# Performance work log

Hardware: AMD Instinct MI355X
Metric: run time of the kernel (lower is better)

Reference implementation:

```python
import jax, jax.numpy as jnp
import numpy as np

N_NODES = 50000
N_EDGES = 800000
IN_FEATS, H_FEATS, N_CLASSES = 64, 64, 16


def setup_inputs() -> dict:
    key = jax.random.key(0)
    ks = jax.random.split(key, 8)
    x = jax.random.normal(ks[0], (N_NODES, IN_FEATS), dtype=jnp.float32)
    src = jax.random.randint(ks[1], (N_EDGES,), 0, N_NODES, dtype=jnp.int64)
    dst = jax.random.randint(ks[2], (N_EDGES,), 0, N_NODES, dtype=jnp.int64)
    W_self1 = jax.random.normal(ks[3], (IN_FEATS, H_FEATS), dtype=jnp.float32) / np.sqrt(IN_FEATS)
    W_neigh1 = jax.random.normal(ks[4], (IN_FEATS, H_FEATS), dtype=jnp.float32) / np.sqrt(IN_FEATS)
    b1 = jnp.zeros((H_FEATS,), dtype=jnp.float32)
    W_self2 = jax.random.normal(ks[5], (H_FEATS, N_CLASSES), dtype=jnp.float32) / np.sqrt(H_FEATS)
    W_neigh2 = jax.random.normal(ks[6], (H_FEATS, N_CLASSES), dtype=jnp.float32) / np.sqrt(H_FEATS)
    b2 = jnp.zeros((N_CLASSES,), dtype=jnp.float32)
    return {"x": x, "src": src, "dst": dst,
            "W_self1": W_self1, "W_neigh1": W_neigh1, "b1": b1,
            "W_self2": W_self2, "W_neigh2": W_neigh2, "b2": b2}


def _mean_agg(h, src, dst, n_nodes):
    # gather source-node features along edges, sum into destinations, divide by in-degree
    summed = jax.ops.segment_sum(h[src], dst, num_segments=n_nodes)  # [N, d]
    deg = jax.ops.segment_sum(jnp.ones_like(src, dtype=h.dtype), dst, num_segments=n_nodes)
    return summed / jnp.maximum(deg, 1.0)[:, None]  # zero in-degree -> zeros (DGL semantics)


def _sage_layer(h, src, dst, W_self, W_neigh, b):
    h_neigh = _mean_agg(h, src, dst, h.shape[0])
    return h @ W_self + h_neigh @ W_neigh + b


def reference(x, src, dst, W_self1, W_neigh1, b1, W_self2, W_neigh2, b2):
    h = _sage_layer(x, src, dst, W_self1, W_neigh1, b1)
    h = jax.nn.relu(h)
    out = _sage_layer(h, src, dst, W_self2, W_neigh2, b2)
    return out
```

## Files before the change

### kernel.cpp

```cpp
#include <hip/hip_runtime.h>
#include <hip/hip_bf16.h>
#include <cstring>


#define FEATS 64
#define CLS   16
#define EPT   16
#define CAP   5120

typedef unsigned short bf16_t;
typedef float floatx2 __attribute__((ext_vector_type(2)));

__device__ __forceinline__ float bfbits2f(unsigned lo16) {
    unsigned v = lo16 << 16;
    float f;
    __builtin_memcpy(&f, &v, 4);
    return f;
}
__device__ __forceinline__ bf16_t f2bf(float f) {
    unsigned u;
    __builtin_memcpy(&u, &f, 4);
    u = (u + 0x7FFFu + ((u >> 16) & 1u)) >> 16;
    return (bf16_t)u;
}
__device__ __forceinline__ unsigned pack2(float a, float b) {
    return (unsigned)f2bf(a) | ((unsigned)f2bf(b) << 16);
}
__device__ __forceinline__ unsigned pack4_fp8(float a, float b, float c, float d) {
    int q = __builtin_amdgcn_cvt_pk_fp8_f32(a, b, 0, false);
    q = __builtin_amdgcn_cvt_pk_fp8_f32(c, d, q, true);
    return (unsigned)q;
}

__global__ __launch_bounds__(256) void fused_pg_kernel(
    const int* __restrict__ src, const int* __restrict__ dst,
    int* __restrict__ bucket_cnt, int* __restrict__ epart, int E,
    const float* __restrict__ x, const float* __restrict__ Ws,
    const float* __restrict__ Wn, bf16_t* __restrict__ selfo,
    unsigned char* __restrict__ t1, int N, int nbp)
{
    __shared__ float smem[16512];
    int t = threadIdx.x;

    if ((int)blockIdx.x < nbp) {
        int* hist = (int*)smem;
        int* base = hist + 256;
        int e0 = blockIdx.x * (256 * EPT);
        hist[t] = 0;
        __syncthreads();
        int pk[EPT];
        int bk[EPT];
#pragma unroll
        for (int j = 0; j < EPT; ++j) {
            int e = e0 + j * 256 + t;
            if (e < E) {
                int d = dst[e];
                pk[j] = (src[e] << 8) | (d & 255);
                bk[j] = d >> 8;
                atomicAdd(&hist[bk[j]], 1);
            } else bk[j] = -1;
        }
        __syncthreads();
        int c = hist[t];
        if (c) base[t] = atomicAdd(&bucket_cnt[t], c);
        hist[t] = 0;
        __syncthreads();
#pragma unroll
        for (int j = 0; j < EPT; ++j) {
            if (bk[j] >= 0) {
                int r = atomicAdd(&hist[bk[j]], 1);
                epart[bk[j] * CAP + base[bk[j]] + r] = pk[j];
            }
        }
        return;
    }

    float* Wc = smem;
    float* xs = smem + 8192;
    int node0 = ((int)blockIdx.x - nbp) * 128;

    for (int idx = t; idx < 64 * 128; idx += 256) {
        int k = idx >> 7, c = idx & 127;
        Wc[idx] = (c < 64) ? Ws[k * 64 + c] : Wn[k * 64 + (c - 64)];
    }
    for (int idx = t; idx < 128 * 16; idx += 256) {
        int row = idx >> 4, c4 = idx & 15;
        int node = node0 + row;
        float4 v = (node < N) ? ((const float4*)(x + (size_t)node * 64))[c4]
                              : make_float4(0.f, 0.f, 0.f, 0.f);
        float* p = &xs[row * 65 + c4 * 4];
        p[0] = v.x; p[1] = v.y; p[2] = v.z; p[3] = v.w;
    }
    __syncthreads();

    int m = t & 31;
    int g = t >> 5;
    float acc[4][16];
#pragma unroll
    for (int j = 0; j < 4; ++j)
#pragma unroll
        for (int c = 0; c < 16; ++c) acc[j][c] = 0.f;

    for (int k = 0; k < 64; ++k) {
        float w[16];
        const float* wp = &Wc[k * 128 + g * 16];
#pragma unroll
        for (int c = 0; c < 16; ++c) w[c] = wp[c];
        float a0 = xs[m * 65 + k];
        float a1 = xs[(m + 32) * 65 + k];
        float a2 = xs[(m + 64) * 65 + k];
        float a3 = xs[(m + 96) * 65 + k];
#pragma unroll
        for (int c = 0; c < 16; ++c) {
            acc[0][c] += a0 * w[c];
            acc[1][c] += a1 * w[c];
            acc[2][c] += a2 * w[c];
            acc[3][c] += a3 * w[c];
        }
    }
#pragma unroll
    for (int j = 0; j < 4; ++j) {
        int node = node0 + m + 32 * j;
        if (node < N) {
            if (g < 4) {
                bf16_t* dstp = selfo + (size_t)node * 64 + g * 16;
                uint4 p0, p1;
                p0.x = pack2(acc[j][0],  acc[j][1]);  p0.y = pack2(acc[j][2],  acc[j][3]);
                p0.z = pack2(acc[j][4],  acc[j][5]);  p0.w = pack2(acc[j][6],  acc[j][7]);
                p1.x = pack2(acc[j][8],  acc[j][9]);  p1.y = pack2(acc[j][10], acc[j][11]);
                p1.z = pack2(acc[j][12], acc[j][13]); p1.w = pack2(acc[j][14], acc[j][15]);
                *(uint4*)(dstp) = p0;
                *(uint4*)(dstp + 8) = p1;
            } else {
                unsigned char* dstp = t1 + (size_t)node * 64 + (g - 4) * 16;
                uint4 q;
                q.x = pack4_fp8(acc[j][0],  acc[j][1],  acc[j][2],  acc[j][3]);
                q.y = pack4_fp8(acc[j][4],  acc[j][5],  acc[j][6],  acc[j][7]);
                q.z = pack4_fp8(acc[j][8],  acc[j][9],  acc[j][10], acc[j][11]);
                q.w = pack4_fp8(acc[j][12], acc[j][13], acc[j][14], acc[j][15]);
                *(uint4*)(dstp) = q;
            }
        }
    }
}

__global__ __launch_bounds__(256) void buildcsr_kernel(const int* __restrict__ epart,
                                                       const int* __restrict__ bucket_cnt,
                                                       int* __restrict__ row_start,
                                                       unsigned short* __restrict__ deg16,
                                                       int* __restrict__ csr, int N) {
    __shared__ int cnt[256];
    __shared__ int pref[256];
    __shared__ int s[256];
    int t = threadIdx.x;
    int b = blockIdx.x;
    int ebeg = b * CAP;
    int ecnt = bucket_cnt[b];
    cnt[t] = 0;
    __syncthreads();
    for (int e = t; e < ecnt; e += 256)
        atomicAdd(&cnt[epart[ebeg + e] & 255], 1);
    __syncthreads();
    int v = cnt[t];
    s[t] = v;
    __syncthreads();
    for (int off = 1; off < 256; off <<= 1) {
        int u = (t >= off) ? s[t - off] : 0;
        __syncthreads();
        s[t] += u;
        __syncthreads();
    }
    pref[t] = s[t] - v;
    int node = b * 256 + t;
    if (node < N) {
        row_start[node] = ebeg + pref[t];
        deg16[node] = (unsigned short)v;
    }
    cnt[t] = 0;
    __syncthreads();
    for (int e = t; e < ecnt; e += 256) {
        int pk = epart[ebeg + e];
        int ln = pk & 255;
        int r = atomicAdd(&cnt[ln], 1);
        csr[ebeg + pref[ln] + r] = pk >> 8;
    }
}

__global__ __launch_bounds__(256) void gather64_kernel(
    const int* __restrict__ csr, const int* __restrict__ row_start,
    const unsigned short* __restrict__ deg16,
    const unsigned char* __restrict__ t1, const bf16_t* __restrict__ selfo,
    bf16_t* __restrict__ h1, const float* __restrict__ b1, int N)
{
    int wid = (blockIdx.x * 256 + threadIdx.x) >> 6;
    int lane = threadIdx.x & 63;
    int eslot = lane >> 4;
    int cg = lane & 15;
    if (wid >= N) return;
    int beg = row_start[wid];
    int d = deg16[wid];
    float ax = 0.f, ay = 0.f, az = 0.f, aw = 0.f;
    int i = eslot;
    for (; i + 12 < d; i += 16) {
        int s0 = csr[beg + i];
        int s1 = csr[beg + i + 4];
        int s2 = csr[beg + i + 8];
        int s3 = csr[beg + i + 12];
        unsigned r0 = *(const unsigned*)(t1 + (size_t)s0 * 64 + cg * 4);
        unsigned r1 = *(const unsigned*)(t1 + (size_t)s1 * 64 + cg * 4);
        unsigned r2 = *(const unsigned*)(t1 + (size_t)s2 * 64 + cg * 4);
        unsigned r3 = *(const unsigned*)(t1 + (size_t)s3 * 64 + cg * 4);
        floatx2 p0 = __builtin_amdgcn_cvt_pk_f32_fp8((int)r0, false);
        floatx2 q0 = __builtin_amdgcn_cvt_pk_f32_fp8((int)r0, true);
        floatx2 p1 = __builtin_amdgcn_cvt_pk_f32_fp8((int)r1, false);
        floatx2 q1 = __builtin_amdgcn_cvt_pk_f32_fp8((int)r1, true);
        floatx2 p2 = __builtin_amdgcn_cvt_pk_f32_fp8((int)r2, false);
        floatx2 q2 = __builtin_amdgcn_cvt_pk_f32_fp8((int)r2, true);
        floatx2 p3 = __builtin_amdgcn_cvt_pk_f32_fp8((int)r3, false);
        floatx2 q3 = __builtin_amdgcn_cvt_pk_f32_fp8((int)r3, true);
        ax += p0.x + p1.x + p2.x + p3.x;
        ay += p0.y + p1.y + p2.y + p3.y;
        az += q0.x + q1.x + q2.x + q3.x;
        aw += q0.y + q1.y + q2.y + q3.y;
    }
    for (; i < d; i += 4) {
        int s0 = csr[beg + i];
        unsigned r0 = *(const unsigned*)(t1 + (size_t)s0 * 64 + cg * 4);
        floatx2 p0 = __builtin_amdgcn_cvt_pk_f32_fp8((int)r0, false);
        floatx2 q0 = __builtin_amdgcn_cvt_pk_f32_fp8((int)r0, true);
        ax += p0.x; ay += p0.y; az += q0.x; aw += q0.y;
    }
    ax += __shfl_xor(ax, 16); ay += __shfl_xor(ay, 16);
    az += __shfl_xor(az, 16); aw += __shfl_xor(aw, 16);
    ax += __shfl_xor(ax, 32); ay += __shfl_xor(ay, 32);
    az += __shfl_xor(az, 32); aw += __shfl_xor(aw, 32);
    if (eslot == 0) {
        float inv = 1.f / fmaxf((float)d, 1.f);
        size_t o = (size_t)wid * 64 + cg * 4;
        uint2 su = *(const uint2*)(selfo + o);
        float4 bb = *(const float4*)(b1 + cg * 4);
        float rx = fmaxf(bfbits2f(su.x & 0xffff) + ax * inv + bb.x, 0.f);
        float ry = fmaxf(bfbits2f(su.x >> 16)    + ay * inv + bb.y, 0.f);
        float rz = fmaxf(bfbits2f(su.y & 0xffff) + az * inv + bb.z, 0.f);
        float rw = fmaxf(bfbits2f(su.y >> 16)    + aw * inv + bb.w, 0.f);
        uint2 pk;
        pk.x = pack2(rx, ry);
        pk.y = pack2(rz, rw);
        *(uint2*)(h1 + o) = pk;
    }
}

__global__ __launch_bounds__(256) void gemm2_kernel(
    const bf16_t* __restrict__ h1, const float* __restrict__ Ws,
    const float* __restrict__ Wn, float* __restrict__ outp,
    bf16_t* __restrict__ t2, int N)
{
    __shared__ float Wc[64 * 32];
    __shared__ float xs[128 * 65];
    int t = threadIdx.x;
    int node0 = blockIdx.x * 128;

    for (int idx = t; idx < 64 * 32; idx += 256) {
        int k = idx >> 5, c = idx & 31;
        Wc[idx] = (c < 16) ? Ws[k * 16 + c] : Wn[k * 16 + (c - 16)];
    }
    for (int idx = t; idx < 128 * 8; idx += 256) {
        int row = idx >> 3, c8 = idx & 7;
        int node = node0 + row;
        float* p = &xs[row * 65 + c8 * 8];
        if (node < N) {
            uint4 u = *(const uint4*)(h1 + (size_t)node * 64 + c8 * 8);
            p[0] = bfbits2f(u.x & 0xffff); p[1] = bfbits2f(u.x >> 16);
            p[2] = bfbits2f(u.y & 0xffff); p[3] = bfbits2f(u.y >> 16);
            p[4] = bfbits2f(u.z & 0xffff); p[5] = bfbits2f(u.z >> 16);
            p[6] = bfbits2f(u.w & 0xffff); p[7] = bfbits2f(u.w >> 16);
        } else {
            for (int qq = 0; qq < 8; ++qq) p[qq] = 0.f;
        }
    }
    __syncthreads();

    int m = t & 31;
    int g = t >> 5;
    float acc[4][4];
#pragma unroll
    for (int j = 0; j < 4; ++j)
#pragma unroll
        for (int c = 0; c < 4; ++c) acc[j][c] = 0.f;

    for (int k = 0; k < 64; ++k) {
        float w[4];
        const float* wp = &Wc[k * 32 + g * 4];
#pragma unroll
        for (int c = 0; c < 4; ++c) w[c] = wp[c];
        float a0 = xs[m * 65 + k];
        float a1 = xs[(m + 32) * 65 + k];
        float a2 = xs[(m + 64) * 65 + k];
        float a3 = xs[(m + 96) * 65 + k];
#pragma unroll
        for (int c = 0; c < 4; ++c) {
            acc[0][c] += a0 * w[c];
            acc[1][c] += a1 * w[c];
            acc[2][c] += a2 * w[c];
            acc[3][c] += a3 * w[c];
        }
    }
#pragma unroll
    for (int j = 0; j < 4; ++j) {
        int node = node0 + m + 32 * j;
        if (node < N) {
            if (g < 4) {
                *(float4*)(outp + (size_t)node * 16 + g * 4) =
                    make_float4(acc[j][0], acc[j][1], acc[j][2], acc[j][3]);
            } else {
                uint2 pk;
                pk.x = pack2(acc[j][0], acc[j][1]);
                pk.y = pack2(acc[j][2], acc[j][3]);
                *(uint2*)(t2 + (size_t)node * 16 + (g - 4) * 4) = pk;
            }
        }
    }
}

__global__ __launch_bounds__(256) void gather16_kernel(
    const int* __restrict__ csr, const int* __restrict__ row_start,
    const unsigned short* __restrict__ deg16,
    const bf16_t* __restrict__ t2,
    float* __restrict__ outp, const float* __restrict__ b2, int N)
{
    int gt = blockIdx.x * 256 + threadIdx.x;
    int node = gt >> 3;
    int c2 = gt & 7;
    if (node >= N) return;
    int beg = row_start[node];
    int d = deg16[node];
    int end = beg + d;
    float a0 = 0.f, a1 = 0.f;
    int i = beg;
    for (; i + 4 <= end; i += 4) {
        int s0 = csr[i], s1 = csr[i + 1], s2 = csr[i + 2], s3 = csr[i + 3];
        unsigned u0 = *(const unsigned*)(t2 + (size_t)s0 * 16 + c2 * 2);
        unsigned u1 = *(const unsigned*)(t2 + (size_t)s1 * 16 + c2 * 2);
        unsigned u2 = *(const unsigned*)(t2 + (size_t)s2 * 16 + c2 * 2);
        unsigned u3 = *(const unsigned*)(t2 + (size_t)s3 * 16 + c2 * 2);
        a0 += bfbits2f(u0 & 0xffff) + bfbits2f(u1 & 0xffff)
            + bfbits2f(u2 & 0xffff) + bfbits2f(u3 & 0xffff);
        a1 += bfbits2f(u0 >> 16) + bfbits2f(u1 >> 16)
            + bfbits2f(u2 >> 16) + bfbits2f(u3 >> 16);
    }
    for (; i < end; ++i) {
        int s = csr[i];
        unsigned u = *(const unsigned*)(t2 + (size_t)s * 16 + c2 * 2);
        a0 += bfbits2f(u & 0xffff);
        a1 += bfbits2f(u >> 16);
    }
    float inv = 1.f / fmaxf((float)d, 1.f);
    size_t o = (size_t)node * 16 + c2 * 2;
    outp[o]     += a0 * inv + b2[c2 * 2];
    outp[o + 1] += a1 * inv + b2[c2 * 2 + 1];
}

extern "C" void kernel_launch(void* const* d_in, const int* in_sizes, int n_in,
                              void* d_out, int out_size, void* d_ws, size_t ws_size,
                              hipStream_t stream) {
    const float* x   = (const float*)d_in[0];
    const int*   src = (const int*)d_in[1];
    const int*   dst = (const int*)d_in[2];
    const float* Ws1 = (const float*)d_in[3];
    const float* Wn1 = (const float*)d_in[4];
    const float* b1  = (const float*)d_in[5];
    const float* Ws2 = (const float*)d_in[6];
    const float* Wn2 = (const float*)d_in[7];
    const float* b2  = (const float*)d_in[8];
    float* outp = (float*)d_out;

    const int N = in_sizes[0] / FEATS;
    const int E = in_sizes[1];
    const int B = (N + 255) / 256;
    const int NBP = (E + 256 * EPT - 1) / (256 * EPT);
    const int NBG = (N + 127) / 128;

    char* p = (char*)d_ws;
    auto align16 = [](char* q) { return (char*)(((size_t)q + 15) & ~(size_t)15); };
    int* bucket_cnt    = (int*)p;                  p = (char*)(bucket_cnt + 256);
    int* epart         = (int*)p;                  p = (char*)(epart + (size_t)B * CAP);
    int* csr           = (int*)p;                  p = (char*)(csr + (size_t)B * CAP);
    int* row_start     = (int*)align16(p);         p = (char*)(row_start + N);
    unsigned short* deg16 = (unsigned short*)align16(p); p = (char*)(deg16 + N);
    bf16_t* selfo      = (bf16_t*)align16(p);      p = (char*)(selfo + (size_t)N * 64);
    unsigned char* t1  = (unsigned char*)align16(p); p = (char*)(t1 + (size_t)N * 64);
    bf16_t* h1         = (bf16_t*)align16(p);      p = (char*)(h1 + (size_t)N * 64);
    bf16_t* t2         = (bf16_t*)align16(p);

    hipMemsetAsync(bucket_cnt, 0, 256 * sizeof(int), stream);

    fused_pg_kernel<<<NBP + NBG, 256, 0, stream>>>(
        src, dst, bucket_cnt, epart, E, x, Ws1, Wn1, selfo, t1, N, NBP);
    buildcsr_kernel<<<B, 256, 0, stream>>>(epart, bucket_cnt, row_start, deg16, csr, N);

    gather64_kernel<<<((size_t)N * 64 + 255) / 256, 256, 0, stream>>>(
        csr, row_start, deg16, t1, selfo, h1, b1, N);
    gemm2_kernel<<<(N + 127) / 128, 256, 0, stream>>>(h1, Ws2, Wn2, outp, t2, N);
    gather16_kernel<<<((size_t)N * 8 + 255) / 256, 256, 0, stream>>>(
        csr, row_start, deg16, t2, outp, b2, N);
}
```

Measured before the change: 159.4 us.

## Branchless degree-specialized gathers and wavefront-per-node layer-2 aggregation

gather64 now handles degrees up to 16 and up to 32 with fully unrolled, clamped-index loads that are masked by a multiplier. This removes loop overhead and exposes all loads at once, since average in-degree is about 16. The self and bias loads are hoisted ahead of the gather so their latency overlaps it. gather16 is rewritten from 8 threads per node to a full 64-lane wavefront per node, with 8 edge slots and a shuffle reduction. That launches 8x more threads and leaves many lanes idle on the epilogue, in exchange for more memory-level parallelism.

Measured after the change: 155.0 us. 1.03x faster.

```diff
diff --git a/kernel.cpp b/kernel.cpp
--- a/kernel.cpp
+++ b/kernel.cpp
@@ -199,46 +199,87 @@
     if (wid >= N) return;
     int beg = row_start[wid];
     int d = deg16[wid];
+    size_t o = (size_t)wid * 64 + cg * 4;
+    uint2 su;
+    float4 bb;
+    if (eslot == 0) {
+        su = *(const uint2*)(selfo + o);
+        bb = *(const float4*)(b1 + cg * 4);
+    }
     float ax = 0.f, ay = 0.f, az = 0.f, aw = 0.f;
-    int i = eslot;
-    for (; i + 12 < d; i += 16) {
-        int s0 = csr[beg + i];
-        int s1 = csr[beg + i + 4];
-        int s2 = csr[beg + i + 8];
-        int s3 = csr[beg + i + 12];
-        unsigned r0 = *(const unsigned*)(t1 + (size_t)s0 * 64 + cg * 4);
-        unsigned r1 = *(const unsigned*)(t1 + (size_t)s1 * 64 + cg * 4);
-        unsigned r2 = *(const unsigned*)(t1 + (size_t)s2 * 64 + cg * 4);
-        unsigned r3 = *(const unsigned*)(t1 + (size_t)s3 * 64 + cg * 4);
-        floatx2 p0 = __builtin_amdgcn_cvt_pk_f32_fp8((int)r0, false);
-        floatx2 q0 = __builtin_amdgcn_cvt_pk_f32_fp8((int)r0, true);
-        floatx2 p1 = __builtin_amdgcn_cvt_pk_f32_fp8((int)r1, false);
-        floatx2 q1 = __builtin_amdgcn_cvt_pk_f32_fp8((int)r1, true);
-        floatx2 p2 = __builtin_amdgcn_cvt_pk_f32_fp8((int)r2, false);
-        floatx2 q2 = __builtin_amdgcn_cvt_pk_f32_fp8((int)r2, true);
-        floatx2 p3 = __builtin_amdgcn_cvt_pk_f32_fp8((int)r3, false);
-        floatx2 q3 = __builtin_amdgcn_cvt_pk_f32_fp8((int)r3, true);
-        ax += p0.x + p1.x + p2.x + p3.x;
-        ay += p0.y + p1.y + p2.y + p3.y;
-        az += q0.x + q1.x + q2.x + q3.x;
-        aw += q0.y + q1.y + q2.y + q3.y;
-    }
-    for (; i < d; i += 4) {
-        int s0 = csr[beg + i];
-        unsigned r0 = *(const unsigned*)(t1 + (size_t)s0 * 64 + cg * 4);
-        floatx2 p0 = __builtin_amdgcn_cvt_pk_f32_fp8((int)r0, false);
-        floatx2 q0 = __builtin_amdgcn_cvt_pk_f32_fp8((int)r0, true);
-        ax += p0.x; ay += p0.y; az += q0.x; aw += q0.y;
-    }
-    ax += __shfl_xor(ax, 16); ay += __shfl_xor(ay, 16);
-    az += __shfl_xor(az, 16); aw += __shfl_xor(aw, 16);
-    ax += __shfl_xor(ax, 32); ay += __shfl_xor(ay, 32);
-    az += __shfl_xor(az, 32); aw += __shfl_xor(aw, 32);
+    if (d > 0) {
+        int dm1 = d - 1;
+#define G64_ACC(r, m)                                                    \
+        {                                                                \
+            floatx2 p_ = __builtin_amdgcn_cvt_pk_f32_fp8((int)(r), false); \
+            floatx2 q_ = __builtin_amdgcn_cvt_pk_f32_fp8((int)(r), true);  \
+            ax += (m) * p_.x; ay += (m) * p_.y;                          \
+            az += (m) * q_.x; aw += (m) * q_.y;                          \
+        }
+        if (d <= 16) {
+            int i0 = eslot, i1 = eslot + 4, i2 = eslot + 8, i3 = eslot + 12;
+            int j0 = i0 > dm1 ? dm1 : i0;
+            int j1 = i1 > dm1 ? dm1 : i1;
+            int j2 = i2 > dm1 ? dm1 : i2;
+            int j3 = i3 > dm1 ? dm1 : i3;
+            int s0 = csr[beg + j0];
+            int s1 = csr[beg + j1];
+            int s2 = csr[beg + j2];
+            int s3 = csr[beg + j3];
+            unsigned r0 = *(const unsigned*)(t1 + (size_t)s0 * 64 + cg * 4);
+            unsigned r1 = *(const unsigned*)(t1 + (size_t)s1 * 64 + cg * 4);
+            unsigned r2 = *(const unsigned*)(t1 + (size_t)s2 * 64 + cg * 4);
+            unsigned r3 = *(const unsigned*)(t1 + (size_t)s3 * 64 + cg * 4);
+            float m0 = (i0 <= dm1) ? 1.f : 0.f;
+            float m1 = (i1 <= dm1) ? 1.f : 0.f;
+            float m2 = (i2 <= dm1) ? 1.f : 0.f;
+            float m3 = (i3 <= dm1) ? 1.f : 0.f;
+            G64_ACC(r0, m0); G64_ACC(r1, m1); G64_ACC(r2, m2); G64_ACC(r3, m3);
+        } else if (d <= 32) {
+            int idx[8];
+            float mk[8];
+            int ss[8];
+            unsigned rr[8];
+#pragma unroll
+            for (int k = 0; k < 8; ++k) {
+                int i = eslot + 4 * k;
+                idx[k] = i > dm1 ? dm1 : i;
+                mk[k] = (i <= dm1) ? 1.f : 0.f;
+            }
+#pragma unroll
+            for (int k = 0; k < 8; ++k) ss[k] = csr[beg + idx[k]];
+#pragma unroll
+            for (int k = 0; k < 8; ++k)
+                rr[k] = *(const unsigned*)(t1 + (size_t)ss[k] * 64 + cg * 4);
+#pragma unroll
+            for (int k = 0; k < 8; ++k) G64_ACC(rr[k], mk[k]);
+        } else {
+            int i = eslot;
+            for (; i + 12 < d; i += 16) {
+                int s0 = csr[beg + i];
+                int s1 = csr[beg + i + 4];
+                int s2 = csr[beg + i + 8];
+                int s3 = csr[beg + i + 12];
+                unsigned r0 = *(const unsigned*)(t1 + (size_t)s0 * 64 + cg * 4);
+                unsigned r1 = *(const unsigned*)(t1 + (size_t)s1 * 64 + cg * 4);
+                unsigned r2 = *(const unsigned*)(t1 + (size_t)s2 * 64 + cg * 4);
+                unsigned r3 = *(const unsigned*)(t1 + (size_t)s3 * 64 + cg * 4);
+                G64_ACC(r0, 1.f); G64_ACC(r1, 1.f); G64_ACC(r2, 1.f); G64_ACC(r3, 1.f);
+            }
+            for (; i < d; i += 4) {
+                int s0 = csr[beg + i];
+                unsigned r0 = *(const unsigned*)(t1 + (size_t)s0 * 64 + cg * 4);
+                G64_ACC(r0, 1.f);
+            }
+        }
+#undef G64_ACC
+        ax += __shfl_xor(ax, 16); ay += __shfl_xor(ay, 16);
+        az += __shfl_xor(az, 16); aw += __shfl_xor(aw, 16);
+        ax += __shfl_xor(ax, 32); ay += __shfl_xor(ay, 32);
+        az += __shfl_xor(az, 32); aw += __shfl_xor(aw, 32);
+    }
     if (eslot == 0) {
         float inv = 1.f / fmaxf((float)d, 1.f);
-        size_t o = (size_t)wid * 64 + cg * 4;
-        uint2 su = *(const uint2*)(selfo + o);
-        float4 bb = *(const float4*)(b1 + cg * 4);
         float rx = fmaxf(bfbits2f(su.x & 0xffff) + ax * inv + bb.x, 0.f);
         float ry = fmaxf(bfbits2f(su.x >> 16)    + ay * inv + bb.y, 0.f);
         float rz = fmaxf(bfbits2f(su.y & 0xffff) + az * inv + bb.z, 0.f);
@@ -247,6 +288,82 @@
         pk.x = pack2(rx, ry);
         pk.y = pack2(rz, rw);
         *(uint2*)(h1 + o) = pk;
+    }
+}
+
+__global__ __launch_bounds__(256) void gather16_kernel(
+    const int* __restrict__ csr, const int* __restrict__ row_start,
+    const unsigned short* __restrict__ deg16,
+    const bf16_t* __restrict__ t2,
+    float* __restrict__ outp, const float* __restrict__ b2, int N)
+{
+    int wid = (blockIdx.x * 256 + threadIdx.x) >> 6;
+    int lane = threadIdx.x & 63;
+    int eslot = lane >> 3;
+    int c2 = lane & 7;
+    if (wid >= N) return;
+    int beg = row_start[wid];
+    int d = deg16[wid];
+    size_t o = (size_t)wid * 16 + c2 * 2;
+    float o0 = 0.f, o1 = 0.f, bb0 = 0.f, bb1 = 0.f;
+    if (eslot == 0) {
+        o0 = outp[o];
+        o1 = outp[o + 1];
+        bb0 = b2[c2 * 2];
+        bb1 = b2[c2 * 2 + 1];
+    }
+    float a0 = 0.f, a1 = 0.f;
+    if (d > 0) {
+        int dm1 = d - 1;
+        if (d <= 16) {
+            int i0 = eslot, i1 = eslot + 8;
+            int j0 = i0 > dm1 ? dm1 : i0;
+            int j1 = i1 > dm1 ? dm1 : i1;
+            int s0 = csr[beg + j0];
+            int s1 = csr[beg + j1];
+            unsigned u0 = *(const unsigned*)(t2 + (size_t)s0 * 16 + c2 * 2);
+            unsigned u1 = *(const unsigned*)(t2 + (size_t)s1 * 16 + c2 * 2);
+            float m0 = (i0 <= dm1) ? 1.f : 0.f;
+            float m1 = (i1 <= dm1) ? 1.f : 0.f;
+            a0 = m0 * bfbits2f(u0 & 0xffff) + m1 * bfbits2f(u1 & 0xffff);
+            a1 = m0 * bfbits2f(u0 >> 16)    + m1 * bfbits2f(u1 >> 16);
+        } else if (d <= 32) {
+            int idx[4];
+            float mk[4];
+            int ss[4];
+            unsigned uu[4];
+#pragma unroll
+            for (int k = 0; k < 4; ++k) {
+                int i = eslot + 8 * k;
+                idx[k] = i > dm1 ? dm1 : i;
+                mk[k] = (i <= dm1) ? 1.f : 0.f;
+            }
+#pragma unroll
+            for (int k = 0; k < 4; ++k) ss[k] = csr[beg + idx[k]];
+#pragma unroll
+            for (int k = 0; k < 4; ++k)
+                uu[k] = *(const unsigned*)(t2 + (size_t)ss[k] * 16 + c2 * 2);
+#pragma unroll
+            for (int k = 0; k < 4; ++k) {
+                a0 += mk[k] * bfbits2f(uu[k] & 0xffff);
+                a1 += mk[k] * bfbits2f(uu[k] >> 16);
+            }
+        } else {
+            for (int i = eslot; i < d; i += 8) {
+                int s = csr[beg + i];
+                unsigned u = *(const unsigned*)(t2 + (size_t)s * 16 + c2 * 2);
+                a0 += bfbits2f(u & 0xffff);
+                a1 += bfbits2f(u >> 16);
+            }
+        }
+        a0 += __shfl_xor(a0, 8);  a1 += __shfl_xor(a1, 8);
+        a0 += __shfl_xor(a0, 16); a1 += __shfl_xor(a1, 16);
+        a0 += __shfl_xor(a0, 32); a1 += __shfl_xor(a1, 32);
+    }
+    if (eslot == 0) {
+        float inv = 1.f / fmaxf((float)d, 1.f);
+        outp[o]     = o0 + a0 * inv + bb0;
+        outp[o + 1] = o1 + a1 * inv + bb1;
     }
 }
 
@@ -320,44 +437,6 @@
             }
         }
     }
-}
-
-__global__ __launch_bounds__(256) void gather16_kernel(
-    const int* __restrict__ csr, const int* __restrict__ row_start,
-    const unsigned short* __restrict__ deg16,
-    const bf16_t* __restrict__ t2,
-    float* __restrict__ outp, const float* __restrict__ b2, int N)
-{
-    int gt = blockIdx.x * 256 + threadIdx.x;
-    int node = gt >> 3;
-    int c2 = gt & 7;
-    if (node >= N) return;
-    int beg = row_start[node];
-    int d = deg16[node];
-    int end = beg + d;
-    float a0 = 0.f, a1 = 0.f;
-    int i = beg;
-    for (; i + 4 <= end; i += 4) {
-        int s0 = csr[i], s1 = csr[i + 1], s2 = csr[i + 2], s3 = csr[i + 3];
-        unsigned u0 = *(const unsigned*)(t2 + (size_t)s0 * 16 + c2 * 2);
-        unsigned u1 = *(const unsigned*)(t2 + (size_t)s1 * 16 + c2 * 2);
-        unsigned u2 = *(const unsigned*)(t2 + (size_t)s2 * 16 + c2 * 2);
-        unsigned u3 = *(const unsigned*)(t2 + (size_t)s3 * 16 + c2 * 2);
-        a0 += bfbits2f(u0 & 0xffff) + bfbits2f(u1 & 0xffff)
-            + bfbits2f(u2 & 0xffff) + bfbits2f(u3 & 0xffff);
-        a1 += bfbits2f(u0 >> 16) + bfbits2f(u1 >> 16)
-            + bfbits2f(u2 >> 16) + bfbits2f(u3 >> 16);
-    }
-    for (; i < end; ++i) {
-        int s = csr[i];
-        unsigned u = *(const unsigned*)(t2 + (size_t)s * 16 + c2 * 2);
-        a0 += bfbits2f(u & 0xffff);
-        a1 += bfbits2f(u >> 16);
-    }
-    float inv = 1.f / fmaxf((float)d, 1.f);
-    size_t o = (size_t)node * 16 + c2 * 2;
-    outp[o]     += a0 * inv + b2[c2 * 2];
-    outp[o + 1] += a1 * inv + b2[c2 * 2 + 1];
 }
 
 extern "C" void kernel_launch(void* const* d_in, const int* in_sizes, int n_in,
@@ -401,6 +480,6 @@
     gather64_kernel<<<((size_t)N * 64 + 255) / 256, 256, 0, stream>>>(
         csr, row_start, deg16, t1, selfo, h1, b1, N);
     gemm2_kernel<<<(N + 127) / 128, 256, 0, stream>>>(h1, Ws2, Wn2, outp, t2, N);
-    gather16_kernel<<<((size_t)N * 8 + 255) / 256, 256, 0, stream>>>(
+    gather16_kernel<<<((size_t)N * 64 + 255) / 256, 256, 0, stream>>>(
         csr, row_start, deg16, t2, outp, b2, N);
 }
```
